# Kernel tuning notes

Measured on AMD Instinct MI355X. Metric: run time of the kernel, lower is better.

The kernel has to match this reference:

```python
import jax, jax.numpy as jnp
import numpy as np

B, N, K = 16, 1024, 512          # batch, num_clients, max selected
DIN, H, NH, L = 64, 256, 8, 2    # input_dim, hidden_dim, num_heads, num_layers
HD = H // NH
FF = 4 * H
TOTAL_BW = 100.0


def setup_inputs() -> dict:
    key = jax.random.key(0)
    ks = jax.random.split(key, 16)
    p = lambda k, shape: (jax.random.normal(k, shape) * 0.02).astype(jnp.float32)
    x = jax.random.normal(ks[0], (B, N, DIN), dtype=jnp.float32)
    # selected indices: distinct valid prefix (from a permutation), sentinel N afterwards
    perm_keys = jax.random.split(ks[1], B)
    idx = jax.vmap(lambda k: jax.random.permutation(k, N)[:K])(perm_keys)
    lengths = jax.random.randint(ks[2], (B,), K // 2, K + 1)
    idx = jnp.where(jnp.arange(K)[None, :] < lengths[:, None], idx, N).astype(jnp.int32)
    return dict(
        x=x, selected_indices=idx,
        W_in=p(ks[3], (DIN, H)), b_in=jnp.zeros((H,), jnp.float32),
        Wqkv=p(ks[4], (L, H, 3 * H)), bqkv=jnp.zeros((L, 3 * H), jnp.float32),
        Wo=p(ks[5], (L, H, H)), bo=jnp.zeros((L, H), jnp.float32),
        ln1_g=jnp.ones((L, H), jnp.float32), ln1_b=jnp.zeros((L, H), jnp.float32),
        W1=p(ks[6], (L, H, FF)), b1=jnp.zeros((L, FF), jnp.float32),
        W2=p(ks[7], (L, FF, H)), b2=jnp.zeros((L, H), jnp.float32),
        ln2_g=jnp.ones((L, H), jnp.float32), ln2_b=jnp.zeros((L, H), jnp.float32),
        Wc=p(ks[8], (H, H)), bc=jnp.zeros((H,), jnp.float32),
    )


def _layer_norm(x, g, b):
    m = x.mean(-1, keepdims=True)
    v = ((x - m) ** 2).mean(-1, keepdims=True)
    return (x - m) * jax.lax.rsqrt(v + 1e-5) * g + b


def _encoder(x, W_in, b_in, Wqkv, bqkv, Wo, bo, ln1_g, ln1_b, W1, b1, W2, b2, ln2_g, ln2_b):
    h = x @ W_in + b_in  # [B, N, H]
    for l in range(L):
        qkv = h @ Wqkv[l] + bqkv[l]
        q, k, v = jnp.split(qkv, 3, axis=-1)
        q = q.reshape(B, N, NH, HD)
        k = k.reshape(B, N, NH, HD)
        v = v.reshape(B, N, NH, HD)
        scores = jnp.einsum('bqhd,bkhd->bhqk', q, k) / np.float32(np.sqrt(HD))
        a = jax.nn.softmax(scores, axis=-1)
        o = jnp.einsum('bhqk,bkhd->bqhd', a, v).reshape(B, N, H)
        h = _layer_norm(h + o @ Wo[l] + bo[l], ln1_g[l], ln1_b[l])
        f = jax.nn.relu(h @ W1[l] + b1[l]) @ W2[l] + b2[l]
        h = _layer_norm(h + f, ln2_g[l], ln2_b[l])
    return h


def _allocate(enc, idx, Wc, bc):
    # ragged gather: indices >= N are end-markers (valid indices form a prefix)
    mask = idx < N                                   # [B, K] bool
    idx_c = jnp.clip(idx, 0, N - 1)
    g = jnp.take_along_axis(enc, idx_c[..., None].astype(jnp.int32), axis=1)  # [B, K, H]
    g = g * mask[..., None]
    cnt = jnp.maximum(mask.sum(-1, keepdims=True), 1).astype(enc.dtype)      # [B, 1]
    mean = g.sum(1) / cnt                            # [B, H]
    ctx = mean @ Wc + bc                             # [B, H] global context (query)
    scores = jnp.einsum('bh,bkh->bk', ctx, g)        # tiny per-sample attention
    scores = jnp.where(mask, scores, -1e9)
    raw = jax.nn.softmax(scores, axis=-1) * mask * TOTAL_BW
    alloc = jnp.round(raw)                           # rounded integer bandwidths
    diff = TOTAL_BW - alloc.sum(-1)                  # fix rounding so total == 100
    alloc = alloc.at[:, 0].add(diff * mask[:, 0])
    alloc = alloc * mask
    # scatter back to [B, num_clients]; sentinel index N is out-of-bounds -> dropped
    scat_idx = jnp.where(mask, idx_c, N)
    bw = jnp.zeros((B, N), enc.dtype).at[jnp.arange(B)[:, None], scat_idx].set(alloc, mode='drop')
    return bw


def reference(x, selected_indices, W_in, b_in, Wqkv, bqkv, Wo, bo, ln1_g, ln1_b,
              W1, b1, W2, b2, ln2_g, ln2_b, Wc, bc):
    enc = _encoder(x, W_in, b_in, Wqkv, bqkv, Wo, bo, ln1_g, ln1_b, W1, b1, W2, b2, ln2_g, ln2_b)
    bw = _allocate(enc, selected_indices, Wc, bc)
    return (selected_indices, bw)
```

## Files before the change

### kernel.cpp

```cpp
#include <hip/hip_runtime.h>
#include <math.h>

#define BB 16
#define NN 1024
#define KSEL 512
#define DIN 64
#define HH 256
#define NHEAD 8
#define HD 32
#define LL 2
#define FFD 1024
#define MTOT (BB*NN)

typedef __attribute__((ext_vector_type(8))) short s8v;
typedef __attribute__((ext_vector_type(4))) short s4v;
typedef __attribute__((ext_vector_type(4))) float f4v;
typedef __attribute__((ext_vector_type(16))) float f16x;

#define QK_SCALE 0.25503485f

__device__ __forceinline__ float b2f(short u) {
    union { unsigned int i; float f; } v;
    v.i = ((unsigned int)(unsigned short)u) << 16;
    return v.f;
}
__device__ __forceinline__ short f2b(float f) {
    union { float f; unsigned int i; } v;
    v.f = f;
    unsigned int r = v.i + 0x7fffu + ((v.i >> 16) & 1u);
    return (short)(r >> 16);
}
__device__ __forceinline__ unsigned cvtpk_bf16(float a, float b) {
    unsigned r;
    asm("v_cvt_pk_bf16_f32 %0, %1, %2" : "=v"(r) : "v"(a), "v"(b));
    return r;
}

#define GLOAD16(g, l) __builtin_amdgcn_global_load_lds( \
    (const __attribute__((address_space(1))) unsigned int*)(const void*)(g), \
    (__attribute__((address_space(3))) unsigned int*)(l), 16, 0, 0)

__device__ __forceinline__ float block_sum(float v, float* red) {
    #pragma unroll
    for (int o = 32; o; o >>= 1) v += __shfl_down(v, o, 64);
    int wid = threadIdx.x >> 6;
    __syncthreads();
    if ((threadIdx.x & 63) == 0) red[wid] = v;
    __syncthreads();
    return red[0] + red[1] + red[2] + red[3];
}
__device__ __forceinline__ float block_max(float v, float* red) {
    #pragma unroll
    for (int o = 32; o; o >>= 1) v = fmaxf(v, __shfl_down(v, o, 64));
    int wid = threadIdx.x >> 6;
    __syncthreads();
    if ((threadIdx.x & 63) == 0) red[wid] = v;
    __syncthreads();
    return fmaxf(fmaxf(red[0], red[1]), fmaxf(red[2], red[3]));
}

__global__ __launch_bounds__(256) void cvt_kernel(const float* __restrict__ in,
                                                  short* __restrict__ out, int n4) {
    int i = blockIdx.x * 256 + threadIdx.x;
    if (i >= n4) return;
    f4v v = *(const f4v*)(in + (size_t)i * 4);
    s4v o;
    o[0] = f2b(v[0]); o[1] = f2b(v[1]); o[2] = f2b(v[2]); o[3] = f2b(v[3]);
    *(s4v*)(out + (size_t)i * 4) = o;
}

struct WtDesc {
    const float* src[9];
    short* dst[9];
    int K[9], N[9], tb[9];
};
__global__ __launch_bounds__(256) void wtrans_all(WtDesc d) {
    __shared__ float s[32][33];
    const int bid = blockIdx.x;
    int si = 0;
    #pragma unroll
    for (int i = 1; i < 9; ++i) si = (bid >= d.tb[i]) ? i : si;
    const float* in = d.src[si];
    short* out = d.dst[si];
    const int K = d.K[si], N = d.N[si];
    const int lt = bid - d.tb[si];
    const int tn = N >> 5;
    const int bk = (lt / tn) * 32, bn = (lt % tn) * 32;
    const int c = threadIdx.x & 31, r8 = threadIdx.x >> 5;
    #pragma unroll
    for (int i = 0; i < 4; ++i) {
        int r = r8 + i * 8;
        s[r][c] = in[(size_t)(bk + r) * N + bn + c];
    }
    __syncthreads();
    #pragma unroll
    for (int i = 0; i < 4; ++i) {
        int r = r8 + i * 8;
        out[(size_t)(bn + r) * K + bk + c] = f2b(s[c][r]);
    }
}

template<int BN, int RELU, int QSCALE>
__global__ __launch_bounds__(256) void gemm_mfma(const short* __restrict__ A,
                                                 const short* __restrict__ BT,
                                                 const float* __restrict__ bias,
                                                 short* __restrict__ C,
                                                 int M, int K, int N,
                                                 int nbx, int cpx) {
    __shared__ __align__(16) short Alds[128 * 64];
    __shared__ __align__(16) short Blds[BN * 64];
    const int tid = threadIdx.x, lane = tid & 63, wid = tid >> 6;
    const int wg = blockIdx.x;
    const int lid = (wg & 7) * cpx + (wg >> 3);
    const int bx = lid % nbx, by = lid / nbx;
    const int bm = by * 128, bn = bx * BN;
    const int wr = wid >> 1, wc = wid & 1;
    const int NF = BN / 32;
    f4v acc[4][NF] = {};

    const short* aB = A + (size_t)bm * K;
    const short* bB = BT + (size_t)bn * K;
    const int frow = lane & 15, fs = lane >> 4;

    for (int k0 = 0; k0 < K; k0 += 64) {
        #pragma unroll
        for (int i = 0; i < 4; ++i) {
            int cb = wid * 64 + i * 256;
            int c = cb + lane;
            int row = c >> 3;
            GLOAD16(aB + (size_t)row * K + k0 + (((c & 7) ^ (row & 7)) * 8), Alds + cb * 8);
        }
        #pragma unroll
        for (int i = 0; i < NF; ++i) {
            int cb = wid * 64 + i * 256;
            int c = cb + lane;
            int row = c >> 3;
            GLOAD16(bB + (size_t)row * K + k0 + (((c & 7) ^ (row & 7)) * 8), Blds + cb * 8);
        }
        __syncthreads();
        #pragma unroll
        for (int kk = 0; kk < 2; ++kk) {
            s8v af[4], bf[NF];
            #pragma unroll
            for (int m = 0; m < 4; ++m) {
                int row = wr * 64 + m * 16 + frow;
                af[m] = *(const s8v*)(Alds + row * 64 + (((kk * 4 + fs) ^ (row & 7)) * 8));
            }
            #pragma unroll
            for (int n = 0; n < NF; ++n) {
                int row = wc * (BN / 2) + n * 16 + frow;
                bf[n] = *(const s8v*)(Blds + row * 64 + (((kk * 4 + fs) ^ (row & 7)) * 8));
            }
            __builtin_amdgcn_s_setprio(1);
            #pragma unroll
            for (int m = 0; m < 4; ++m)
                #pragma unroll
                for (int n = 0; n < NF; ++n)
                    acc[m][n] = __builtin_amdgcn_mfma_f32_16x16x32_bf16(af[m], bf[n], acc[m][n], 0, 0, 0);
            __builtin_amdgcn_s_setprio(0);
        }
        __syncthreads();
    }
    #pragma unroll
    for (int m = 0; m < 4; ++m) {
        int rbase = bm + wr * 64 + m * 16 + (lane >> 4) * 4;
        #pragma unroll
        for (int n = 0; n < NF; ++n) {
            int col = bn + wc * (BN / 2) + n * 16 + (lane & 15);
            float bv = bias[col];
            #pragma unroll
            for (int r = 0; r < 4; ++r) {
                float v = acc[m][n][r] + bv;
                if (QSCALE) { if (col < 256) v *= QK_SCALE; }
                if (RELU) v = fmaxf(v, 0.f);
                C[(size_t)(rbase + r) * N + col] = f2b(v);
            }
        }
    }
}

__global__ __launch_bounds__(512) void attn_mfma(const short* __restrict__ qkv,
                                                 short* __restrict__ o) {
    __shared__ __align__(16) short Klds[2][4][128][8];
    __shared__ __align__(16) short Vlds[2][32][136];
    const int tid = threadIdx.x, lane = tid & 63, wid = tid >> 6;
    const int hi = lane >> 5, lq = lane & 31;
    const int wg = blockIdx.x;
    const int lid = (wg & 7) * 64 + (wg >> 3);
    const int qt = lid & 3;
    const int h  = (lid >> 2) & 7;
    const int b  = lid >> 5;
    const int q0 = qt * 256 + wid * 32;
    const short* qkvb = qkv + (size_t)b * NN * 768;

    s8v qf0, qf1;
    {
        const short* qrow = qkvb + (size_t)(q0 + lq) * 768 + h * 32 + hi * 8;
        qf0 = *(const s8v*)qrow;
        qf1 = *(const s8v*)(qrow + 16);
    }

    const int token = tid & 127, cK = tid >> 7, dc = cK * 8;
    const f16x fz = {};

    float l = 0.f;
    f16x acc = {};

    {
        const short* kvrow = qkvb + (size_t)token * 768 + 256 + h * 32;
        GLOAD16(kvrow + cK * 8, &Klds[0][cK][token][0]);
        s8v vv = *(const s8v*)(kvrow + 256 + dc);
        #pragma unroll
        for (int j = 0; j < 8; ++j) Vlds[0][dc + j][token] = vv[j];
    }
    __syncthreads();

    for (int t = 0; t < 8; ++t) {
        const int bb = t & 1;
        s8v vvn;
        if (t < 7) {
            const short* kvrow = qkvb + (size_t)((t + 1) * 128 + token) * 768 + 256 + h * 32;
            GLOAD16(kvrow + cK * 8, &Klds[bb ^ 1][cK][token][0]);
            vvn = *(const s8v*)(kvrow + 256 + dc);
        }
        #pragma unroll
        for (int kt = 0; kt < 4; ++kt) {
            const s8v kf0 = *(const s8v*)&Klds[bb][hi][kt * 32 + lq][0];
            const s8v kf1 = *(const s8v*)&Klds[bb][2 + hi][kt * 32 + lq][0];
            __builtin_amdgcn_s_setprio(1);
            f16x p = __builtin_amdgcn_mfma_f32_32x32x16_bf16(kf0, qf0, fz, 0, 0, 0);
            p = __builtin_amdgcn_mfma_f32_32x32x16_bf16(kf1, qf1, p, 0, 0, 0);
            __builtin_amdgcn_s_setprio(0);
            float l0 = 0.f, l1 = 0.f, l2 = 0.f, l3 = 0.f;
            #pragma unroll
            for (int r = 0; r < 16; r += 4) {
                p[r]     = __builtin_amdgcn_exp2f(p[r]);     l0 += p[r];
                p[r + 1] = __builtin_amdgcn_exp2f(p[r + 1]); l1 += p[r + 1];
                p[r + 2] = __builtin_amdgcn_exp2f(p[r + 2]); l2 += p[r + 2];
                p[r + 3] = __builtin_amdgcn_exp2f(p[r + 3]); l3 += p[r + 3];
            }
            l += (l0 + l1) + (l2 + l3);
            unsigned w[8];
            #pragma unroll
            for (int i = 0; i < 8; ++i) w[i] = cvtpk_bf16(p[2 * i], p[2 * i + 1]);
            asm volatile("v_permlane32_swap_b32 %0, %1" : "+v"(w[0]), "+v"(w[2]));
            asm volatile("v_permlane32_swap_b32 %0, %1" : "+v"(w[1]), "+v"(w[3]));
            asm volatile("v_permlane32_swap_b32 %0, %1" : "+v"(w[4]), "+v"(w[6]));
            asm volatile("v_permlane32_swap_b32 %0, %1" : "+v"(w[5]), "+v"(w[7]));
            union { unsigned u[4]; s8v v; } pa0, pa1;
            pa0.u[0] = w[0]; pa0.u[1] = w[1]; pa0.u[2] = w[2]; pa0.u[3] = w[3];
            pa1.u[0] = w[4]; pa1.u[1] = w[5]; pa1.u[2] = w[6]; pa1.u[3] = w[7];
            const s8v vf0 = *(const s8v*)&Vlds[bb][lq][kt * 32 + hi * 8];
            const s8v vf1 = *(const s8v*)&Vlds[bb][lq][kt * 32 + 16 + hi * 8];
            __builtin_amdgcn_s_setprio(1);
            acc = __builtin_amdgcn_mfma_f32_32x32x16_bf16(pa0.v, vf0, acc, 0, 0, 0);
            acc = __builtin_amdgcn_mfma_f32_32x32x16_bf16(pa1.v, vf1, acc, 0, 0, 0);
            __builtin_amdgcn_s_setprio(0);
        }
        if (t < 7) {
            #pragma unroll
            for (int j = 0; j < 8; ++j) Vlds[bb ^ 1][dc + j][token] = vvn[j];
        }
        __syncthreads();
    }

    l += __shfl_xor(l, 32);
    float inv = 1.f / l;
    short* ob = o + ((size_t)(b * NN + q0)) * HH + h * 32 + lq;
    #pragma unroll
    for (int r = 0; r < 16; ++r) {
        int qr = (r & 3) + 8 * (r >> 2) + 4 * hi;
        float invr = __shfl(inv, qr);
        ob[(size_t)qr * HH] = f2b(acc[r] * invr);
    }
}

__global__ __launch_bounds__(256) void ln_residual_kernel(short* __restrict__ hio,
                                                          const short* __restrict__ delta,
                                                          const float* __restrict__ g,
                                                          const float* __restrict__ bta) {
    const int w = threadIdx.x >> 6, lane = threadIdx.x & 63;
    const size_t row = (size_t)blockIdx.x * 4 + w;
    const int c0 = lane * 4;
    s4v hv = *(const s4v*)(hio + row * HH + c0);
    s4v dv = *(const s4v*)(delta + row * HH + c0);
    float v[4];
    float ps = 0.f;
    #pragma unroll
    for (int i = 0; i < 4; ++i) { v[i] = b2f(hv[i]) + b2f(dv[i]); ps += v[i]; }
    #pragma unroll
    for (int o = 32; o; o >>= 1) ps += __shfl_xor(ps, o);
    float mean = ps * (1.f / HH);
    float pv = 0.f;
    #pragma unroll
    for (int i = 0; i < 4; ++i) { v[i] -= mean; pv += v[i] * v[i]; }
    #pragma unroll
    for (int o = 32; o; o >>= 1) pv += __shfl_xor(pv, o);
    float rs = rsqrtf(pv * (1.f / HH) + 1e-5f);
    const f4v gv = *(const f4v*)(g + c0);
    const f4v bv = *(const f4v*)(bta + c0);
    s4v ov;
    #pragma unroll
    for (int i = 0; i < 4; ++i) ov[i] = f2b(v[i] * rs * gv[i] + bv[i]);
    *(s4v*)(hio + row * HH + c0) = ov;
}

__global__ __launch_bounds__(256) void alloc_mean_part(const short* __restrict__ enc,
                                                       const int* __restrict__ idx,
                                                       float* __restrict__ psum) {
    __shared__ int ids[32];
    const int b = blockIdx.x >> 4, s = blockIdx.x & 15;
    const int t = threadIdx.x;
    if (t < 32) ids[t] = idx[b * KSEL + s * 32 + t];
    __syncthreads();
    float sum = 0.f;
    #pragma unroll
    for (int i = 0; i < 32; ++i) {
        int id = ids[i];
        if (id < NN) sum += b2f(enc[(size_t)(b * NN + id) * HH + t]);
    }
    psum[(size_t)blockIdx.x * HH + t] = sum;
}

__global__ __launch_bounds__(256) void alloc_ctx(const float* __restrict__ psum,
                                                 const int* __restrict__ idx,
                                                 const float* __restrict__ Wc,
                                                 const float* __restrict__ bc,
                                                 float* __restrict__ ctxg) {
    __shared__ float mean_s[HH];
    __shared__ float red[4];
    const int b = blockIdx.x, t = threadIdx.x;
    int i0 = idx[b * KSEL + t], i1 = idx[b * KSEL + 256 + t];
    float c = (i0 < NN ? 1.f : 0.f) + (i1 < NN ? 1.f : 0.f);
    float cnt = fmaxf(block_sum(c, red), 1.f);
    float s = 0.f;
    #pragma unroll
    for (int p = 0; p < 16; ++p) s += psum[(size_t)(b * 16 + p) * HH + t];
    mean_s[t] = s / cnt;
    __syncthreads();
    float cv = bc[t];
    #pragma unroll 8
    for (int j = 0; j < HH; ++j) cv = fmaf(mean_s[j], Wc[(size_t)j * HH + t], cv);
    ctxg[b * HH + t] = cv;
}

__global__ __launch_bounds__(256) void alloc_scores(const short* __restrict__ enc,
                                                    const int* __restrict__ idx,
                                                    const float* __restrict__ ctxg,
                                                    float* __restrict__ scores) {
    const int b = blockIdx.x >> 3, s = blockIdx.x & 7;
    const int t = threadIdx.x, lane = t & 63, w = t >> 6;
    const f4v cv = *(const f4v*)(ctxg + b * HH + lane * 4);
    #pragma unroll 4
    for (int i = 0; i < 16; ++i) {
        int k = s * 64 + w * 16 + i;
        int id = idx[b * KSEL + k];
        float sc = -1e9f;
        if (id < NN) {
            s4v v = *(const s4v*)(enc + (size_t)(b * NN + id) * HH + lane * 4);
            float p = cv[0] * b2f(v[0]) + cv[1] * b2f(v[1]) + cv[2] * b2f(v[2]) + cv[3] * b2f(v[3]);
            #pragma unroll
            for (int o = 32; o; o >>= 1) p += __shfl_xor(p, o);
            sc = p;
        }
        if (lane == 0) scores[b * KSEL + k] = sc;
    }
}

__global__ __launch_bounds__(256) void alloc_final(const int* __restrict__ idx,
                                                   const float* __restrict__ scores,
                                                   float* __restrict__ out) {
    __shared__ float alloc_s[KSEL];
    __shared__ float red[4];
    __shared__ float diff_s;
    const int b = blockIdx.x, t = threadIdx.x;
    int i0 = idx[b * KSEL + t], i1 = idx[b * KSEL + 256 + t];
    float s0 = scores[b * KSEL + t], s1 = scores[b * KSEL + 256 + t];
    float smax = block_max(fmaxf(s0, s1), red);
    float e0 = (i0 < NN) ? __expf(s0 - smax) : 0.f;
    float e1 = (i1 < NN) ? __expf(s1 - smax) : 0.f;
    float ssum = block_sum(e0 + e1, red);
    float inv = 100.f / ssum;
    float a0 = rintf(e0 * inv);
    float a1 = rintf(e1 * inv);
    alloc_s[t] = a0;
    alloc_s[t + 256] = a1;
    float asum = block_sum(a0 + a1, red);
    if (t == 0) diff_s = 100.f - asum;
    __syncthreads();
    if (t == 0 && i0 < NN) alloc_s[0] += diff_s;
    __syncthreads();

    float* bw = out + BB * KSEL + (size_t)b * NN;
    #pragma unroll
    for (int n = t; n < NN; n += 256) bw[n] = 0.f;
    __syncthreads();
    out[b * KSEL + t] = (float)i0;
    out[b * KSEL + 256 + t] = (float)i1;
    if (i0 < NN) bw[i0] = alloc_s[t];
    if (i1 < NN) bw[i1] = alloc_s[t + 256];
}

extern "C" void kernel_launch(void* const* d_in, const int* in_sizes, int n_in,
                              void* d_out, int out_size, void* d_ws, size_t ws_size,
                              hipStream_t stream) {
    const float* x     = (const float*)d_in[0];
    const int*   sel   = (const int*)  d_in[1];
    const float* W_in  = (const float*)d_in[2];
    const float* b_in  = (const float*)d_in[3];
    const float* Wqkv  = (const float*)d_in[4];
    const float* bqkv  = (const float*)d_in[5];
    const float* Wo    = (const float*)d_in[6];
    const float* bo    = (const float*)d_in[7];
    const float* ln1_g = (const float*)d_in[8];
    const float* ln1_b = (const float*)d_in[9];
    const float* W1    = (const float*)d_in[10];
    const float* b1    = (const float*)d_in[11];
    const float* W2    = (const float*)d_in[12];
    const float* b2    = (const float*)d_in[13];
    const float* ln2_g = (const float*)d_in[14];
    const float* ln2_b = (const float*)d_in[15];
    const float* Wc    = (const float*)d_in[16];
    const float* bc    = (const float*)d_in[17];
    float* out = (float*)d_out;

    char* base = (char*)d_ws;
    short* h    = (short*)(base);
    short* qkv  = (short*)(base + (8u << 20));
    short* obuf = (short*)(base + (32u << 20));
    short* ff   = (short*)(base + (40u << 20));
    short* xb   = (short*)(base + (76u << 20));
    short* wt   = (short*)(base + (78u << 20));
    short* W_inT  = wt;
    short* WqkvT  = W_inT + 256 * 64;
    short* WoT    = WqkvT + LL * 768 * 256;
    short* W1T    = WoT   + LL * 256 * 256;
    short* W2T    = W1T   + LL * 1024 * 256;

    float* psum   = (float*)(base + (40u << 20));
    float* ctxg   = psum + BB * 16 * HH;
    float* scores = ctxg + BB * HH;

    cvt_kernel<<<(MTOT * DIN / 4 + 255) / 256, 256, 0, stream>>>(x, xb, MTOT * DIN / 4);

    {
        WtDesc d;
        const float* srcs[9] = { W_in, Wqkv, Wqkv + (size_t)HH * 768, Wo, Wo + (size_t)HH * HH,
                                 W1, W1 + (size_t)HH * FFD, W2, W2 + (size_t)FFD * HH };
        short* dsts[9] = { W_inT, WqkvT, WqkvT + 768 * 256, WoT, WoT + 256 * 256,
                           W1T, W1T + 1024 * 256, W2T, W2T + 256 * 1024 };
        int Ks[9] = { 64, 256, 256, 256, 256, 256, 256, 1024, 1024 };
        int Ns[9] = { 256, 768, 768, 256, 256, 1024, 1024, 256, 256 };
        int tb = 0;
        for (int i = 0; i < 9; ++i) {
            d.src[i] = srcs[i]; d.dst[i] = dsts[i];
            d.K[i] = Ks[i]; d.N[i] = Ns[i]; d.tb[i] = tb;
            tb += (Ks[i] >> 5) * (Ns[i] >> 5);
        }
        wtrans_all<<<tb, 256, 0, stream>>>(d);
    }

    gemm_mfma<64,0,0><<<512, 256, 0, stream>>>(xb, W_inT, b_in, h, MTOT, DIN, HH, 4, 64);

    for (int l = 0; l < LL; ++l) {
        gemm_mfma<128,0,1><<<768, 256, 0, stream>>>(
            h, WqkvT + (size_t)l * 768 * HH, bqkv + l * 768, qkv, MTOT, HH, 768, 6, 96);
        attn_mfma<<<BB * NHEAD * 4, 512, 0, stream>>>(qkv, obuf);
        gemm_mfma<64,0,0><<<512, 256, 0, stream>>>(
            obuf, WoT + (size_t)l * HH * HH, bo + l * HH, qkv, MTOT, HH, HH, 4, 64);
        ln_residual_kernel<<<MTOT / 4, 256, 0, stream>>>(h, qkv, ln1_g + l * HH, ln1_b + l * HH);
        gemm_mfma<128,1,0><<<1024, 256, 0, stream>>>(
            h, W1T + (size_t)l * FFD * HH, b1 + l * FFD, ff, MTOT, HH, FFD, 8, 128);
        gemm_mfma<64,0,0><<<512, 256, 0, stream>>>(
            ff, W2T + (size_t)l * HH * FFD, b2 + l * HH, qkv, MTOT, FFD, HH, 4, 64);
        ln_residual_kernel<<<MTOT / 4, 256, 0, stream>>>(h, qkv, ln2_g + l * HH, ln2_b + l * HH);
    }

    alloc_mean_part<<<BB * 16, 256, 0, stream>>>(h, sel, psum);
    alloc_ctx<<<BB, 256, 0, stream>>>(psum, sel, Wc, bc, ctxg);
    alloc_scores<<<BB * 8, 256, 0, stream>>>(h, sel, ctxg, scores);
    alloc_final<<<BB, 256, 0, stream>>>(sel, scores, out);
}
```

Measured before the change: 353.6 us.

## Fuse output GEMMs with residual LayerNorm and merge small allocator kernels

Adds a gemm_ln kernel that computes the Wo and W2 projections on full 256-column row tiles. It adds the residual, computes LayerNorm statistics in registers and LDS, and writes h in place, which removes the intermediate buffer round trip and the separate ln_residual launches. The x conversion is folded into the weight-transpose launch, and the four allocator kernels are merged into one 1024-thread block per batch. The cost is fewer blocks for the output GEMMs (256 blocks of 64 rows) with a larger LDS footprint, and a variance computed as E[x^2]-mean^2, which is less numerically stable.

After: 329.1 us. 1.07x faster.

```diff
diff --git a/kernel.cpp b/kernel.cpp
--- a/kernel.cpp
+++ b/kernel.cpp
@@ -40,43 +40,25 @@
     (const __attribute__((address_space(1))) unsigned int*)(const void*)(g), \
     (__attribute__((address_space(3))) unsigned int*)(l), 16, 0, 0)
 
-__device__ __forceinline__ float block_sum(float v, float* red) {
-    #pragma unroll
-    for (int o = 32; o; o >>= 1) v += __shfl_down(v, o, 64);
-    int wid = threadIdx.x >> 6;
-    __syncthreads();
-    if ((threadIdx.x & 63) == 0) red[wid] = v;
-    __syncthreads();
-    return red[0] + red[1] + red[2] + red[3];
-}
-__device__ __forceinline__ float block_max(float v, float* red) {
-    #pragma unroll
-    for (int o = 32; o; o >>= 1) v = fmaxf(v, __shfl_down(v, o, 64));
-    int wid = threadIdx.x >> 6;
-    __syncthreads();
-    if ((threadIdx.x & 63) == 0) red[wid] = v;
-    __syncthreads();
-    return fmaxf(fmaxf(red[0], red[1]), fmaxf(red[2], red[3]));
-}
-
-__global__ __launch_bounds__(256) void cvt_kernel(const float* __restrict__ in,
-                                                  short* __restrict__ out, int n4) {
-    int i = blockIdx.x * 256 + threadIdx.x;
-    if (i >= n4) return;
-    f4v v = *(const f4v*)(in + (size_t)i * 4);
-    s4v o;
-    o[0] = f2b(v[0]); o[1] = f2b(v[1]); o[2] = f2b(v[2]); o[3] = f2b(v[3]);
-    *(s4v*)(out + (size_t)i * 4) = o;
-}
-
 struct WtDesc {
     const float* src[9];
     short* dst[9];
     int K[9], N[9], tb[9];
+    const float* x;
+    short* xb;
+    int cvt_tb;
 };
 __global__ __launch_bounds__(256) void wtrans_all(WtDesc d) {
     __shared__ float s[32][33];
     const int bid = blockIdx.x;
+    if (bid >= d.cvt_tb) {
+        int i = (bid - d.cvt_tb) * 256 + threadIdx.x;
+        f4v v = *(const f4v*)(d.x + (size_t)i * 4);
+        s4v o;
+        o[0] = f2b(v[0]); o[1] = f2b(v[1]); o[2] = f2b(v[2]); o[3] = f2b(v[3]);
+        *(s4v*)(d.xb + (size_t)i * 4) = o;
+        return;
+    }
     int si = 0;
     #pragma unroll
     for (int i = 1; i < 9; ++i) si = (bid >= d.tb[i]) ? i : si;
@@ -179,6 +161,134 @@
     }
 }
 
+__global__ __launch_bounds__(256) void gemm_ln(const short* __restrict__ A,
+                                               const short* __restrict__ BT,
+                                               const float* __restrict__ bias,
+                                               short* __restrict__ h,
+                                               const float* __restrict__ g,
+                                               const float* __restrict__ beta,
+                                               int K) {
+    __shared__ __align__(16) short Alds[2][64 * 64];
+    __shared__ __align__(16) short Blds[2][256 * 64];
+    __shared__ float lred[64][2][2];
+    const int tid = threadIdx.x, lane = tid & 63, wid = tid >> 6;
+    const int wr = wid >> 1, wc = wid & 1;
+    const int bm = blockIdx.x * 64;
+    const int frow = lane & 15, fs = lane >> 4;
+    f4v acc[2][8] = {};
+
+    const short* aB = A + (size_t)bm * K;
+
+    #define STAGE_AB(buf, k0)                                                            \
+        {                                                                                \
+            _Pragma("unroll")                                                            \
+            for (int i = 0; i < 2; ++i) {                                                \
+                int u = i * 256 + tid;                                                   \
+                int row = u >> 3;                                                        \
+                GLOAD16(aB + (size_t)row * K + (k0) + (((u & 7) ^ (row & 7)) * 8),       \
+                        Alds[buf] + u * 8);                                              \
+            }                                                                            \
+            _Pragma("unroll")                                                            \
+            for (int i = 0; i < 8; ++i) {                                                \
+                int u = i * 256 + tid;                                                   \
+                int row = u >> 3;                                                        \
+                GLOAD16(BT + (size_t)row * K + (k0) + (((u & 7) ^ (row & 7)) * 8),       \
+                        Blds[buf] + u * 8);                                              \
+            }                                                                            \
+        }
+
+    STAGE_AB(0, 0);
+    __syncthreads();
+    int cur = 0;
+    for (int k0 = 0; k0 < K; k0 += 64) {
+        if (k0 + 64 < K) STAGE_AB(cur ^ 1, k0 + 64);
+        #pragma unroll
+        for (int kk = 0; kk < 2; ++kk) {
+            s8v af[2], bf[8];
+            #pragma unroll
+            for (int m = 0; m < 2; ++m) {
+                int row = wr * 32 + m * 16 + frow;
+                af[m] = *(const s8v*)(Alds[cur] + row * 64 + (((kk * 4 + fs) ^ (row & 7)) * 8));
+            }
+            #pragma unroll
+            for (int n = 0; n < 8; ++n) {
+                int row = wc * 128 + n * 16 + frow;
+                bf[n] = *(const s8v*)(Blds[cur] + row * 64 + (((kk * 4 + fs) ^ (row & 7)) * 8));
+            }
+            __builtin_amdgcn_s_setprio(1);
+            #pragma unroll
+            for (int m = 0; m < 2; ++m)
+                #pragma unroll
+                for (int n = 0; n < 8; ++n)
+                    acc[m][n] = __builtin_amdgcn_mfma_f32_16x16x32_bf16(af[m], bf[n], acc[m][n], 0, 0, 0);
+            __builtin_amdgcn_s_setprio(0);
+        }
+        __syncthreads();
+        cur ^= 1;
+    }
+    #undef STAGE_AB
+
+    float s1[2][4], s2[2][4];
+    #pragma unroll
+    for (int m = 0; m < 2; ++m) {
+        #pragma unroll
+        for (int r = 0; r < 4; ++r) { s1[m][r] = 0.f; s2[m][r] = 0.f; }
+    }
+    #pragma unroll
+    for (int m = 0; m < 2; ++m) {
+        #pragma unroll
+        for (int n = 0; n < 8; ++n) {
+            int gc = wc * 128 + n * 16 + frow;
+            float bv = bias[gc];
+            #pragma unroll
+            for (int r = 0; r < 4; ++r) {
+                int gr = bm + wr * 32 + m * 16 + (lane >> 4) * 4 + r;
+                float v = acc[m][n][r] + bv + b2f(h[(size_t)gr * HH + gc]);
+                acc[m][n][r] = v;
+                s1[m][r] += v;
+                s2[m][r] += v * v;
+            }
+        }
+    }
+    #pragma unroll
+    for (int m = 0; m < 2; ++m) {
+        #pragma unroll
+        for (int r = 0; r < 4; ++r) {
+            float a = s1[m][r], bq = s2[m][r];
+            #pragma unroll
+            for (int off = 1; off < 16; off <<= 1) {
+                a += __shfl_xor(a, off);
+                bq += __shfl_xor(bq, off);
+            }
+            s1[m][r] = a; s2[m][r] = bq;
+            if (frow == 0) {
+                int lr = wr * 32 + m * 16 + (lane >> 4) * 4 + r;
+                lred[lr][wc][0] = a;
+                lred[lr][wc][1] = bq;
+            }
+        }
+    }
+    __syncthreads();
+    #pragma unroll
+    for (int m = 0; m < 2; ++m) {
+        #pragma unroll
+        for (int r = 0; r < 4; ++r) {
+            int lr = wr * 32 + m * 16 + (lane >> 4) * 4 + r;
+            float t1 = lred[lr][0][0] + lred[lr][1][0];
+            float t2 = lred[lr][0][1] + lred[lr][1][1];
+            float mean = t1 * (1.f / HH);
+            float var = t2 * (1.f / HH) - mean * mean;
+            float rs = rsqrtf(var + 1e-5f);
+            int gr = bm + lr;
+            #pragma unroll
+            for (int n = 0; n < 8; ++n) {
+                int gc = wc * 128 + n * 16 + frow;
+                h[(size_t)gr * HH + gc] = f2b((acc[m][n][r] - mean) * rs * g[gc] + beta[gc]);
+            }
+        }
+    }
+}
+
 __global__ __launch_bounds__(512) void attn_mfma(const short* __restrict__ qkv,
                                                  short* __restrict__ o) {
     __shared__ __align__(16) short Klds[2][4][128][8];
@@ -275,130 +385,142 @@
     }
 }
 
-__global__ __launch_bounds__(256) void ln_residual_kernel(short* __restrict__ hio,
-                                                          const short* __restrict__ delta,
-                                                          const float* __restrict__ g,
-                                                          const float* __restrict__ bta) {
-    const int w = threadIdx.x >> 6, lane = threadIdx.x & 63;
-    const size_t row = (size_t)blockIdx.x * 4 + w;
-    const int c0 = lane * 4;
-    s4v hv = *(const s4v*)(hio + row * HH + c0);
-    s4v dv = *(const s4v*)(delta + row * HH + c0);
-    float v[4];
-    float ps = 0.f;
-    #pragma unroll
-    for (int i = 0; i < 4; ++i) { v[i] = b2f(hv[i]) + b2f(dv[i]); ps += v[i]; }
-    #pragma unroll
-    for (int o = 32; o; o >>= 1) ps += __shfl_xor(ps, o);
-    float mean = ps * (1.f / HH);
-    float pv = 0.f;
-    #pragma unroll
-    for (int i = 0; i < 4; ++i) { v[i] -= mean; pv += v[i] * v[i]; }
-    #pragma unroll
-    for (int o = 32; o; o >>= 1) pv += __shfl_xor(pv, o);
-    float rs = rsqrtf(pv * (1.f / HH) + 1e-5f);
-    const f4v gv = *(const f4v*)(g + c0);
-    const f4v bv = *(const f4v*)(bta + c0);
-    s4v ov;
-    #pragma unroll
-    for (int i = 0; i < 4; ++i) ov[i] = f2b(v[i] * rs * gv[i] + bv[i]);
-    *(s4v*)(hio + row * HH + c0) = ov;
-}
-
-__global__ __launch_bounds__(256) void alloc_mean_part(const short* __restrict__ enc,
-                                                       const int* __restrict__ idx,
-                                                       float* __restrict__ psum) {
-    __shared__ int ids[32];
-    const int b = blockIdx.x >> 4, s = blockIdx.x & 15;
-    const int t = threadIdx.x;
-    if (t < 32) ids[t] = idx[b * KSEL + s * 32 + t];
-    __syncthreads();
-    float sum = 0.f;
-    #pragma unroll
-    for (int i = 0; i < 32; ++i) {
-        int id = ids[i];
-        if (id < NN) sum += b2f(enc[(size_t)(b * NN + id) * HH + t]);
-    }
-    psum[(size_t)blockIdx.x * HH + t] = sum;
-}
-
-__global__ __launch_bounds__(256) void alloc_ctx(const float* __restrict__ psum,
-                                                 const int* __restrict__ idx,
-                                                 const float* __restrict__ Wc,
-                                                 const float* __restrict__ bc,
-                                                 float* __restrict__ ctxg) {
+__global__ __launch_bounds__(1024) void alloc_all(const short* __restrict__ enc,
+                                                  const int* __restrict__ idx,
+                                                  const float* __restrict__ Wc,
+                                                  const float* __restrict__ bc,
+                                                  float* __restrict__ out) {
+    __shared__ float part[16][HH];
     __shared__ float mean_s[HH];
-    __shared__ float red[4];
+    __shared__ float ctx_s[HH];
+    __shared__ float sc_s[KSEL];
+    __shared__ float alloc_s[KSEL];
+    __shared__ int   idx_s[KSEL];
+    __shared__ float red[16];
+    __shared__ float cnt_s, smax_s, ssum_s, diff_s;
     const int b = blockIdx.x, t = threadIdx.x;
-    int i0 = idx[b * KSEL + t], i1 = idx[b * KSEL + 256 + t];
-    float c = (i0 < NN ? 1.f : 0.f) + (i1 < NN ? 1.f : 0.f);
-    float cnt = fmaxf(block_sum(c, red), 1.f);
-    float s = 0.f;
-    #pragma unroll
-    for (int p = 0; p < 16; ++p) s += psum[(size_t)(b * 16 + p) * HH + t];
-    mean_s[t] = s / cnt;
-    __syncthreads();
-    float cv = bc[t];
-    #pragma unroll 8
-    for (int j = 0; j < HH; ++j) cv = fmaf(mean_s[j], Wc[(size_t)j * HH + t], cv);
-    ctxg[b * HH + t] = cv;
-}
-
-__global__ __launch_bounds__(256) void alloc_scores(const short* __restrict__ enc,
-                                                    const int* __restrict__ idx,
-                                                    const float* __restrict__ ctxg,
-                                                    float* __restrict__ scores) {
-    const int b = blockIdx.x >> 3, s = blockIdx.x & 7;
-    const int t = threadIdx.x, lane = t & 63, w = t >> 6;
-    const f4v cv = *(const f4v*)(ctxg + b * HH + lane * 4);
-    #pragma unroll 4
-    for (int i = 0; i < 16; ++i) {
-        int k = s * 64 + w * 16 + i;
-        int id = idx[b * KSEL + k];
-        float sc = -1e9f;
-        if (id < NN) {
-            s4v v = *(const s4v*)(enc + (size_t)(b * NN + id) * HH + lane * 4);
-            float p = cv[0] * b2f(v[0]) + cv[1] * b2f(v[1]) + cv[2] * b2f(v[2]) + cv[3] * b2f(v[3]);
-            #pragma unroll
-            for (int o = 32; o; o >>= 1) p += __shfl_xor(p, o);
-            sc = p;
-        }
-        if (lane == 0) scores[b * KSEL + k] = sc;
-    }
-}
-
-__global__ __launch_bounds__(256) void alloc_final(const int* __restrict__ idx,
-                                                   const float* __restrict__ scores,
-                                                   float* __restrict__ out) {
-    __shared__ float alloc_s[KSEL];
-    __shared__ float red[4];
-    __shared__ float diff_s;
-    const int b = blockIdx.x, t = threadIdx.x;
-    int i0 = idx[b * KSEL + t], i1 = idx[b * KSEL + 256 + t];
-    float s0 = scores[b * KSEL + t], s1 = scores[b * KSEL + 256 + t];
-    float smax = block_max(fmaxf(s0, s1), red);
-    float e0 = (i0 < NN) ? __expf(s0 - smax) : 0.f;
-    float e1 = (i1 < NN) ? __expf(s1 - smax) : 0.f;
-    float ssum = block_sum(e0 + e1, red);
-    float inv = 100.f / ssum;
-    float a0 = rintf(e0 * inv);
-    float a1 = rintf(e1 * inv);
-    alloc_s[t] = a0;
-    alloc_s[t + 256] = a1;
-    float asum = block_sum(a0 + a1, red);
-    if (t == 0) diff_s = 100.f - asum;
-    __syncthreads();
-    if (t == 0 && i0 < NN) alloc_s[0] += diff_s;
-    __syncthreads();
+    const int w = t >> 6, lane = t & 63;
+
+    if (t < KSEL) idx_s[t] = idx[b * KSEL + t];
+    __syncthreads();
+
+    {
+        float c = (t < KSEL && idx_s[t] < NN) ? 1.f : 0.f;
+        #pragma unroll
+        for (int o = 32; o; o >>= 1) c += __shfl_xor(c, o);
+        if (lane == 0) red[w] = c;
+        __syncthreads();
+        if (t == 0) {
+            float s = 0.f;
+            #pragma unroll
+            for (int i = 0; i < 16; ++i) s += red[i];
+            cnt_s = fmaxf(s, 1.f);
+        }
+    }
+
+    {
+        const int c0 = lane * 4;
+        float s0 = 0.f, s1 = 0.f, s2 = 0.f, s3 = 0.f;
+        #pragma unroll
+        for (int i = 0; i < 32; ++i) {
+            int id = idx_s[w * 32 + i];
+            if (id < NN) {
+                s4v v = *(const s4v*)(enc + (size_t)(b * NN + id) * HH + c0);
+                s0 += b2f(v[0]); s1 += b2f(v[1]); s2 += b2f(v[2]); s3 += b2f(v[3]);
+            }
+        }
+        part[w][c0] = s0; part[w][c0 + 1] = s1; part[w][c0 + 2] = s2; part[w][c0 + 3] = s3;
+    }
+    __syncthreads();
+    if (t < HH) {
+        float s = 0.f;
+        #pragma unroll
+        for (int p = 0; p < 16; ++p) s += part[p][t];
+        mean_s[t] = s / cnt_s;
+    }
+    __syncthreads();
+    if (t < HH) {
+        float cv = bc[t];
+        #pragma unroll 8
+        for (int j = 0; j < HH; ++j) cv = fmaf(mean_s[j], Wc[(size_t)j * HH + t], cv);
+        ctx_s[t] = cv;
+    }
+    __syncthreads();
+
+    {
+        const f4v cv = *(const f4v*)(ctx_s + lane * 4);
+        for (int i = 0; i < 32; ++i) {
+            int k = w * 32 + i;
+            int id = idx_s[k];
+            float sc = -1e9f;
+            if (id < NN) {
+                s4v v = *(const s4v*)(enc + (size_t)(b * NN + id) * HH + lane * 4);
+                float p = cv[0] * b2f(v[0]) + cv[1] * b2f(v[1]) + cv[2] * b2f(v[2]) + cv[3] * b2f(v[3]);
+                #pragma unroll
+                for (int o = 32; o; o >>= 1) p += __shfl_xor(p, o);
+                sc = p;
+            }
+            if (lane == 0) sc_s[k] = sc;
+        }
+    }
+    __syncthreads();
+
+    float myv = (t < KSEL) ? sc_s[t] : -1e9f;
+    {
+        float m = myv;
+        #pragma unroll
+        for (int o = 32; o; o >>= 1) m = fmaxf(m, __shfl_xor(m, o));
+        if (lane == 0) red[w] = m;
+        __syncthreads();
+        if (t == 0) {
+            float mm = red[0];
+            #pragma unroll
+            for (int i = 1; i < 16; ++i) mm = fmaxf(mm, red[i]);
+            smax_s = mm;
+        }
+        __syncthreads();
+    }
+    float e = (t < KSEL && idx_s[t] < NN) ? __expf(myv - smax_s) : 0.f;
+    {
+        float s = e;
+        #pragma unroll
+        for (int o = 32; o; o >>= 1) s += __shfl_xor(s, o);
+        if (lane == 0) red[w] = s;
+        __syncthreads();
+        if (t == 0) {
+            float ss = 0.f;
+            #pragma unroll
+            for (int i = 0; i < 16; ++i) ss += red[i];
+            ssum_s = ss;
+        }
+        __syncthreads();
+    }
+    float a = rintf(e * (100.f / ssum_s));
+    if (t < KSEL) alloc_s[t] = a;
+    {
+        float s = (t < KSEL) ? a : 0.f;
+        #pragma unroll
+        for (int o = 32; o; o >>= 1) s += __shfl_xor(s, o);
+        if (lane == 0) red[w] = s;
+        __syncthreads();
+        if (t == 0) {
+            float ss = 0.f;
+            #pragma unroll
+            for (int i = 0; i < 16; ++i) ss += red[i];
+            diff_s = 100.f - ss;
+        }
+        __syncthreads();
+        if (t == 0 && idx_s[0] < NN) alloc_s[0] += diff_s;
+    }
 
     float* bw = out + BB * KSEL + (size_t)b * NN;
-    #pragma unroll
-    for (int n = t; n < NN; n += 256) bw[n] = 0.f;
-    __syncthreads();
-    out[b * KSEL + t] = (float)i0;
-    out[b * KSEL + 256 + t] = (float)i1;
-    if (i0 < NN) bw[i0] = alloc_s[t];
-    if (i1 < NN) bw[i1] = alloc_s[t + 256];
+    bw[t] = 0.f;
+    __syncthreads();
+    if (t < KSEL) {
+        int id = idx_s[t];
+        out[b * KSEL + t] = (float)id;
+        if (id < NN) bw[id] = alloc_s[t];
+    }
 }
 
 extern "C" void kernel_launch(void* const* d_in, const int* in_sizes, int n_in,
@@ -437,12 +559,6 @@
     short* W1T    = WoT   + LL * 256 * 256;
     short* W2T    = W1T   + LL * 1024 * 256;
 
-    float* psum   = (float*)(base + (40u << 20));
-    float* ctxg   = psum + BB * 16 * HH;
-    float* scores = ctxg + BB * HH;
-
-    cvt_kernel<<<(MTOT * DIN / 4 + 255) / 256, 256, 0, stream>>>(x, xb, MTOT * DIN / 4);
-
     {
         WtDesc d;
         const float* srcs[9] = { W_in, Wqkv, Wqkv + (size_t)HH * 768, Wo, Wo + (size_t)HH * HH,
@@ -457,7 +573,8 @@
             d.K[i] = Ks[i]; d.N[i] = Ns[i]; d.tb[i] = tb;
             tb += (Ks[i] >> 5) * (Ns[i] >> 5);
         }
-        wtrans_all<<<tb, 256, 0, stream>>>(d);
+        d.x = x; d.xb = xb; d.cvt_tb = tb;
+        wtrans_all<<<tb + MTOT * DIN / 1024, 256, 0, stream>>>(d);
     }
 
     gemm_mfma<64,0,0><<<512, 256, 0, stream>>>(xb, W_inT, b_in, h, MTOT, DIN, HH, 4, 64);
@@ -466,18 +583,13 @@
         gemm_mfma<128,0,1><<<768, 256, 0, stream>>>(
             h, WqkvT + (size_t)l * 768 * HH, bqkv + l * 768, qkv, MTOT, HH, 768, 6, 96);
         attn_mfma<<<BB * NHEAD * 4, 512, 0, stream>>>(qkv, obuf);
-        gemm_mfma<64,0,0><<<512, 256, 0, stream>>>(
-            obuf, WoT + (size_t)l * HH * HH, bo + l * HH, qkv, MTOT, HH, HH, 4, 64);
-        ln_residual_kernel<<<MTOT / 4, 256, 0, stream>>>(h, qkv, ln1_g + l * HH, ln1_b + l * HH);
+        gemm_ln<<<MTOT / 64, 256, 0, stream>>>(
+            obuf, WoT + (size_t)l * HH * HH, bo + l * HH, h, ln1_g + l * HH, ln1_b + l * HH, HH);
         gemm_mfma<128,1,0><<<1024, 256, 0, stream>>>(
             h, W1T + (size_t)l * FFD * HH, b1 + l * FFD, ff, MTOT, HH, FFD, 8, 128);
-        gemm_mfma<64,0,0><<<512, 256, 0, stream>>>(
-            ff, W2T + (size_t)l * HH * FFD, b2 + l * HH, qkv, MTOT, FFD, HH, 4, 64);
-        ln_residual_kernel<<<MTOT / 4, 256, 0, stream>>>(h, qkv, ln2_g + l * HH, ln2_b + l * HH);
-    }
-
-    alloc_mean_part<<<BB * 16, 256, 0, stream>>>(h, sel, psum);
-    alloc_ctx<<<BB, 256, 0, stream>>>(psum, sel, Wc, bc, ctxg);
-    alloc_scores<<<BB * 8, 256, 0, stream>>>(h, sel, ctxg, scores);
-    alloc_final<<<BB, 256, 0, stream>>>(sel, scores, out);
-}
+        gemm_ln<<<MTOT / 64, 256, 0, stream>>>(
+            ff, W2T + (size_t)l * HH * FFD, b2 + l * HH, h, ln2_g + l * HH, ln2_b + l * HH, FFD);
+    }
+
+    alloc_all<<<BB, 1024, 0, stream>>>(h, sel, Wc, bc, out);
+}
```
